# Kernel tuning notes

Measured on AMD Instinct MI355X. Metric: run time of the kernel, lower is better.

## Reference

```python
import jax, jax.numpy as jnp
import numpy as np

N_IN, N_H0, N_H1, N_H2, N_H3, N_OUT = 512, 1024, 1024, 1024, 512, 128
B, T = 128, 512
STD = 0.05


def setup_inputs() -> dict:
    key = jax.random.key(0)
    ks = jax.random.split(key, 7)
    # torch nn.Linear(in, out, bias=False) stores weight as [out, in]
    return {
        "input_spikes": jax.random.uniform(ks[0], (B, T, N_IN), dtype=jnp.float32),
        "W_in_h0": STD * jax.random.normal(ks[1], (N_H0, N_IN), dtype=jnp.float32),
        "W_h0_h1": STD * jax.random.normal(ks[2], (N_H1, N_H0), dtype=jnp.float32),
        "W_h1_h2": STD * jax.random.normal(ks[3], (N_H2, N_H1), dtype=jnp.float32),
        "W_h2_h2": STD * jax.random.normal(ks[4], (N_H2, N_H2), dtype=jnp.float32),
        "W_h2_h3": STD * jax.random.normal(ks[5], (N_H3, N_H2), dtype=jnp.float32),
        "W_h3_out": STD * jax.random.normal(ks[6], (N_OUT, N_H3), dtype=jnp.float32),
    }


def _lif(current, v, alpha, v_th):
    v = alpha * v + current
    s = (v >= v_th).astype(v.dtype)
    return s, v * (1.0 - s)


def reference(input_spikes, W_in_h0, W_h0_h1, W_h1_h2, W_h2_h2, W_h2_h3, W_h3_out):
    b = input_spikes.shape[0]
    dt = input_spikes.dtype
    z = lambda n: jnp.zeros((b, n), dtype=dt)
    # carry: membrane potentials for h0..h3, out, plus recurrent h2 spikes
    init = (z(N_H0), z(N_H1), z(N_H2), z(N_H3), z(N_OUT), z(N_H2))
    xs = jnp.swapaxes(input_spikes, 0, 1)  # [T, B, N_IN]

    def step(carry, x_t):
        v0, v1, v2, v3, vo, s2_prev = carry
        s0, v0 = _lif(x_t @ W_in_h0.T, v0, 0.9, 0.5)
        s1, v1 = _lif(s0 @ W_h0_h1.T, v1, 0.95, 0.5)
        s2, v2 = _lif(s1 @ W_h1_h2.T + s2_prev @ W_h2_h2.T, v2, 0.93, 0.5)
        s3, v3 = _lif(s2 @ W_h2_h3.T, v3, 0.9, 0.5)
        so, vo = _lif(s3 @ W_h3_out.T, vo, 0.82, 0.8)
        return (v0, v1, v2, v3, vo, s2), so

    _, out = jax.lax.scan(step, init, xs)
    output_spikes = jnp.swapaxes(out, 0, 1)  # [B, T, N_OUT]
    spike_counts = output_spikes.sum(axis=1)  # [B, N_OUT]
    return output_spikes, spike_counts
```

## Files before the change

kernel.cpp:

```cpp
#include <hip/hip_runtime.h>
#include <cstddef>


#define NB 128
#define NT 512

enum : size_t {
  OFF_V0   = 0,
  OFF_V1   = OFF_V0 + 131072,
  OFF_V2   = OFF_V1 + 131072,
  OFF_V3   = OFF_V2 + 131072,
  OFF_VO   = OFF_V3 + 65536,
  OFF_CNT  = OFF_VO + 16384,
  OFF_C2A  = OFF_CNT + 16384,
  OFF_BYTE = OFF_C2A + 262144,
  WS_FLOATS = OFF_BYTE + 229376
};
#define BS0 0
#define BS1 262144
#define BS2 524288
#define BS3 786432

__global__ __launch_bounds__(256) void init_kernel(float* __restrict__ wf) {
  size_t i = (size_t)blockIdx.x * blockDim.x + threadIdx.x;
  size_t stride = (size_t)gridDim.x * blockDim.x;
  for (size_t j = i; j < WS_FLOATS; j += stride) wf[j] = 0.0f;
}

template<bool ABYTE>
__device__ __forceinline__ void gemm_core(
    const void* __restrict__ Abase, int Astride,
    const float* __restrict__ W, int K, int fold,
    int bBase, int oBase,
    float (&As)[2][32][34], float (&Ws)[2][32][34],
    float acc[2][2])
{
  const int tid = threadIdx.x;
  const int ldRow = tid >> 3;
  const int ldK   = (tid & 7) << 2;
  const int tb = (tid & 15) << 1;
  const int to = (tid >> 4) << 1;

  const float* Wrow = W + (size_t)(oBase + ldRow) * K + ldK;
  const unsigned char* Abrow = nullptr;
  const float* Afrow = nullptr;
  if (ABYTE) Abrow = (const unsigned char*)Abase + (size_t)(bBase + ldRow) * Astride + ldK;
  else       Afrow = (const float*)Abase + (size_t)(bBase + ldRow) * Astride + ldK;

  const int NKT = K >> 5;

  float pa[4]; float4 pw;
  {
    float c0, c1, c2, c3;
    if (ABYTE) {
      unsigned int u = *(const unsigned int*)(Abrow);
      c0 = (float)(u & 0xff); c1 = (float)((u >> 8) & 0xff);
      c2 = (float)((u >> 16) & 0xff); c3 = (float)(u >> 24);
    } else {
      float4 f = *(const float4*)(Afrow);
      c0 = f.x; c1 = f.y; c2 = f.z; c3 = f.w;
    }
    float4 cw = *(const float4*)(Wrow);
    As[0][ldK + 0][ldRow] = c0; As[0][ldK + 1][ldRow] = c1;
    As[0][ldK + 2][ldRow] = c2; As[0][ldK + 3][ldRow] = c3;
    Ws[0][ldK + 0][ldRow] = cw.x; Ws[0][ldK + 1][ldRow] = cw.y;
    Ws[0][ldK + 2][ldRow] = cw.z; Ws[0][ldK + 3][ldRow] = cw.w;
  }
  if (NKT > 1) {
    if (ABYTE) {
      unsigned int u = *(const unsigned int*)(Abrow + 32);
      pa[0] = (float)(u & 0xff); pa[1] = (float)((u >> 8) & 0xff);
      pa[2] = (float)((u >> 16) & 0xff); pa[3] = (float)(u >> 24);
    } else {
      float4 f = *(const float4*)(Afrow + 32);
      pa[0] = f.x; pa[1] = f.y; pa[2] = f.z; pa[3] = f.w;
    }
    pw = *(const float4*)(Wrow + 32);
  }
  __syncthreads();

  float tot[2][2] = {{0.f, 0.f}, {0.f, 0.f}};
  float pan[2][2] = {{0.f, 0.f}, {0.f, 0.f}};
  int cb = 0;
  for (int kt = 0; kt < NKT; ++kt) {
    float na[4]; float4 nw;
    if (kt + 2 < NKT) {
      const int ko = (kt + 2) << 5;
      if (ABYTE) {
        unsigned int u = *(const unsigned int*)(Abrow + ko);
        na[0] = (float)(u & 0xff); na[1] = (float)((u >> 8) & 0xff);
        na[2] = (float)((u >> 16) & 0xff); na[3] = (float)(u >> 24);
      } else {
        float4 f = *(const float4*)(Afrow + ko);
        na[0] = f.x; na[1] = f.y; na[2] = f.z; na[3] = f.w;
      }
      nw = *(const float4*)(Wrow + ko);
    }
    if (fold && kt == 16) {
#pragma unroll
      for (int i = 0; i < 2; ++i)
#pragma unroll
        for (int j = 0; j < 2; ++j) {
          tot[i][j] = __fadd_rn(tot[i][j], pan[i][j]);
          pan[i][j] = 0.f;
        }
    }
#pragma unroll
    for (int k = 0; k < 32; ++k) {
      const float2 a = *(const float2*)&As[cb][k][tb];
      const float2 w = *(const float2*)&Ws[cb][k][to];
      pan[0][0] = fmaf(a.x, w.x, pan[0][0]);
      pan[0][1] = fmaf(a.x, w.y, pan[0][1]);
      pan[1][0] = fmaf(a.y, w.x, pan[1][0]);
      pan[1][1] = fmaf(a.y, w.y, pan[1][1]);
    }
    if (kt + 1 < NKT) {
      const int nb = cb ^ 1;
      As[nb][ldK + 0][ldRow] = pa[0]; As[nb][ldK + 1][ldRow] = pa[1];
      As[nb][ldK + 2][ldRow] = pa[2]; As[nb][ldK + 3][ldRow] = pa[3];
      Ws[nb][ldK + 0][ldRow] = pw.x; Ws[nb][ldK + 1][ldRow] = pw.y;
      Ws[nb][ldK + 2][ldRow] = pw.z; Ws[nb][ldK + 3][ldRow] = pw.w;
    }
    if (kt + 2 < NKT) { pa[0] = na[0]; pa[1] = na[1]; pa[2] = na[2]; pa[3] = na[3]; pw = nw; }
    __syncthreads();
    cb ^= 1;
  }
#pragma unroll
  for (int i = 0; i < 2; ++i)
#pragma unroll
    for (int j = 0; j < 2; ++j)
      acc[i][j] = __fadd_rn(tot[i][j], pan[i][j]);
}

__global__ __launch_bounds__(256) void phase_kernel(
    const float* __restrict__ x,
    const float* __restrict__ W0, const float* __restrict__ W1,
    const float* __restrict__ W2a, const float* __restrict__ W2b,
    const float* __restrict__ W3, const float* __restrict__ W4,
    float* __restrict__ wf, float* __restrict__ out, int p)
{
  float* cnt = wf + OFF_CNT;
  float* c2a = wf + OFF_C2A;
  unsigned char* sb = (unsigned char*)(wf + OFF_BYTE);
  const int cur = p & 1, prev = cur ^ 1;

  const int blk = blockIdx.x;
  int g, lb, t, K, N, fold;
  if (blk < 128)      { g = 0; lb = blk;       t = p;     K = 512;  N = 1024; fold = 0; }
  else if (blk < 256) { g = 1; lb = blk - 128; t = p - 1; K = 1024; N = 1024; fold = 1; }
  else if (blk < 384) { g = 2; lb = blk - 256; t = p - 2; K = 1024; N = 1024; fold = 1; }
  else if (blk < 512) { g = 3; lb = blk - 384; t = p - 3; K = 1024; N = 1024; fold = 1; }
  else if (blk < 576) { g = 4; lb = blk - 512; t = p - 4; K = 1024; N = 512;  fold = 1; }
  else                { g = 5; lb = blk - 576; t = p - 5; K = 512;  N = 128;  fold = 0; }
  if (t < 0 || t >= NT) return;

  const int ntO = N >> 5;
  const int bBase = (lb / ntO) << 5;
  const int oBase = (lb % ntO) << 5;

  const float* Wm; const void* Ab; int Astride;
  switch (g) {
    case 0: Wm = W0;  Ab = x + (size_t)t * 512;              Astride = NT * 512; break;
    case 1: Wm = W1;  Ab = sb + BS1 - BS1 + (size_t)prev * 131072; Astride = 1024; break;
    case 2: Wm = W2a; Ab = sb + BS1 + (size_t)prev * 131072; Astride = 1024; break;
    case 3: Wm = W2b; Ab = sb + BS2 + (size_t)prev * 131072; Astride = 1024; break;
    case 4: Wm = W3;  Ab = sb + BS2 + (size_t)prev * 131072; Astride = 1024; break;
    default: Wm = W4; Ab = sb + BS3 + (size_t)prev * 65536;  Astride = 512;  break;
  }

  __shared__ float As[2][32][34];
  __shared__ float Ws[2][32][34];
  float acc[2][2];
  if (g == 0) gemm_core<false>(Ab, Astride, Wm, K, fold, bBase, oBase, As, Ws, acc);
  else        gemm_core<true >(Ab, Astride, Wm, K, fold, bBase, oBase, As, Ws, acc);

  const int tid = threadIdx.x;
  const int tb = (tid & 15) << 1;
  const int to = (tid >> 4) << 1;

  if (g == 2) {
    float* dst = c2a + (size_t)cur * 131072;
#pragma unroll
    for (int i = 0; i < 2; ++i) {
      const int b = bBase + tb + i;
      float2 st; st.x = acc[i][0]; st.y = acc[i][1];
      *(float2*)(dst + (size_t)b * 1024 + oBase + to) = st;
    }
    return;
  }

  float alpha, vth = 0.5f;
  float* v; unsigned char* sOut = nullptr;
  switch (g) {
    case 0: alpha = 0.90f; v = wf + OFF_V0; sOut = sb + BS0 + (size_t)cur * 131072; break;
    case 1: alpha = 0.95f; v = wf + OFF_V1; sOut = sb + BS1 + (size_t)cur * 131072; break;
    case 3: alpha = 0.93f; v = wf + OFF_V2; sOut = sb + BS2 + (size_t)cur * 131072; break;
    case 4: alpha = 0.90f; v = wf + OFF_V3; sOut = sb + BS3 + (size_t)cur * 65536;  break;
    default: alpha = 0.82f; vth = 0.8f; v = wf + OFF_VO; break;
  }
  const float* c2aPrev = c2a + (size_t)prev * 131072;

#pragma unroll
  for (int i = 0; i < 2; ++i) {
    const int b = bBase + tb + i;
    int si[2];
#pragma unroll
    for (int j = 0; j < 2; ++j) {
      const int o = oBase + to + j;
      float cin = acc[i][j];
      if (g == 3)
        cin = __fadd_rn(c2aPrev[(size_t)b * 1024 + o], acc[i][j]);
      float* vp = v + (size_t)b * N + o;
      float vv = __fadd_rn(__fmul_rn(alpha, *vp), cin);
      int s = (vv >= vth) ? 1 : 0;
      float sf = (float)s;
      *vp = __fmul_rn(vv, __fsub_rn(1.0f, sf));
      si[j] = s;
      if (g == 5) {
        out[(size_t)b * (NT * 128) + (size_t)t * 128 + o] = sf;
        cnt[b * 128 + o] = __fadd_rn(cnt[b * 128 + o], sf);
      }
    }
    if (g != 5) {
      *(unsigned short*)(sOut + (size_t)b * N + oBase + to) =
          (unsigned short)(si[0] | (si[1] << 8));
    }
  }
}

__global__ __launch_bounds__(256) void fin_kernel(const float* __restrict__ counts,
                                                  float* __restrict__ out) {
  int i = blockIdx.x * blockDim.x + threadIdx.x;
  if (i < 128 * 128) out[(size_t)128 * NT * 128 + i] = counts[i];
}

extern "C" void kernel_launch(void* const* d_in, const int* in_sizes, int n_in,
                              void* d_out, int out_size, void* d_ws, size_t ws_size,
                              hipStream_t stream) {
  const float* x   = (const float*)d_in[0];
  const float* W0  = (const float*)d_in[1];
  const float* W1  = (const float*)d_in[2];
  const float* W2a = (const float*)d_in[3];
  const float* W2b = (const float*)d_in[4];
  const float* W3  = (const float*)d_in[5];
  const float* W4  = (const float*)d_in[6];
  float* wf  = (float*)d_ws;
  float* out = (float*)d_out;

  init_kernel<<<512, 256, 0, stream>>>(wf);
  for (int p = 0; p < NT + 5; ++p) {
    phase_kernel<<<592, 256, 0, stream>>>(x, W0, W1, W2a, W2b, W3, W4, wf, out, p);
  }
  fin_kernel<<<64, 256, 0, stream>>>(wf + OFF_CNT, out);
}
```

Measured before the change: 24.21 ms.

## Replace per-timestep launches with persistent kernel and grid-wide barrier

Replaces the 517 per-phase kernel launches with one persistent 512-block kernel that loops over phases, synchronising all blocks through a flag-based grid barrier in global memory. Membrane potentials and spike counts stay in LDS per thread instead of being read and written to global memory each step. Work is retiled: layer-0 uses 32x64 tiles with the small output layer merged into the same blocks, and the 1024-K GEMMs split K across two 128-thread halves that are reduced in LDS. This removes launch overhead and global state traffic, but depends on all 512 blocks being co-resident, which is checked with an occupancy query before falling back to a multi-launch path.

```diff
diff --git a/kernel.cpp b/kernel.cpp
--- a/kernel.cpp
+++ b/kernel.cpp
@@ -4,6 +4,7 @@
 
 #define NB 128
 #define NT 512
+#define NBLK 512
 
 enum : size_t {
   OFF_V0   = 0,
@@ -14,218 +15,444 @@
   OFF_CNT  = OFF_VO + 16384,
   OFF_C2A  = OFF_CNT + 16384,
   OFF_BYTE = OFF_C2A + 262144,
-  WS_FLOATS = OFF_BYTE + 229376
+  WS_FLOATS = OFF_BYTE + 229376,
+  OFF_ARR  = WS_FLOATS,
+  OFF_FLAGF = OFF_ARR + 8192,
+  WS_TOTAL = OFF_FLAGF + 16
 };
 #define BS0 0
 #define BS1 262144
 #define BS2 524288
 #define BS3 786432
 
+__device__ __forceinline__ void st_u16_agent(unsigned char* p, unsigned short v) {
+  __hip_atomic_store((unsigned short*)p, v, __ATOMIC_RELAXED, __HIP_MEMORY_SCOPE_AGENT);
+}
+__device__ __forceinline__ unsigned long long ld_u64_agent(const unsigned char* p) {
+  return __hip_atomic_load((const unsigned long long*)p, __ATOMIC_RELAXED, __HIP_MEMORY_SCOPE_AGENT);
+}
+__device__ __forceinline__ void st_u64_agent(void* p, unsigned long long v) {
+  __hip_atomic_store((unsigned long long*)p, v, __ATOMIC_RELAXED, __HIP_MEMORY_SCOPE_AGENT);
+}
+__device__ __forceinline__ unsigned long long ld_u64_agentf(const float* p) {
+  return __hip_atomic_load((const unsigned long long*)p, __ATOMIC_RELAXED, __HIP_MEMORY_SCOPE_AGENT);
+}
+__device__ __forceinline__ unsigned ld_u32_agent(const unsigned* p) {
+  return __hip_atomic_load(p, __ATOMIC_RELAXED, __HIP_MEMORY_SCOPE_AGENT);
+}
+__device__ __forceinline__ void st_u32_agent(unsigned* p, unsigned v) {
+  __hip_atomic_store(p, v, __ATOMIC_RELAXED, __HIP_MEMORY_SCOPE_AGENT);
+}
+
+union F2U { float2 f; unsigned long long u; };
+
+__device__ __forceinline__ void unpack8(unsigned long long v, float* f) {
+  unsigned lo = (unsigned)v, hi = (unsigned)(v >> 32);
+  f[0] = (float)(lo & 0xff); f[1] = (float)((lo >> 8) & 0xff);
+  f[2] = (float)((lo >> 16) & 0xff); f[3] = (float)(lo >> 24);
+  f[4] = (float)(hi & 0xff); f[5] = (float)((hi >> 8) & 0xff);
+  f[6] = (float)((hi >> 16) & 0xff); f[7] = (float)(hi >> 24);
+}
+
+__device__ __forceinline__ void gemm_split32(
+    const unsigned char* __restrict__ Abase,
+    const float* __restrict__ W,
+    int bBase, int oBase, int grp, int lt,
+    float* AsG, float* WsG, float acc[4][2])
+{
+  const int ar = lt >> 2, ac = (lt & 3) << 3;
+  const int wr = lt >> 2, wk = (lt & 3) << 3;
+  const int tb4 = (lt >> 4) << 2;
+  const int to2 = (lt & 15) << 1;
+  const int kb = grp << 9;
+
+  const unsigned char* Arow = Abase + (size_t)(bBase + ar) * 1024 + kb + ac;
+  const float* Wr = W + (size_t)(oBase + wr) * 1024 + kb + wk;
+
+  {
+    float a[8]; unpack8(ld_u64_agent(Arow), a);
+    float4 w0 = *(const float4*)(Wr);
+    float4 w1 = *(const float4*)(Wr + 4);
+#pragma unroll
+    for (int i = 0; i < 8; ++i) AsG[(ac + i) * 32 + ar] = a[i];
+    WsG[(wk+0)*36+wr] = w0.x; WsG[(wk+1)*36+wr] = w0.y;
+    WsG[(wk+2)*36+wr] = w0.z; WsG[(wk+3)*36+wr] = w0.w;
+    WsG[(wk+4)*36+wr] = w1.x; WsG[(wk+5)*36+wr] = w1.y;
+    WsG[(wk+6)*36+wr] = w1.z; WsG[(wk+7)*36+wr] = w1.w;
+  }
+  unsigned long long pa = ld_u64_agent(Arow + 32);
+  float4 pw0 = *(const float4*)(Wr + 32);
+  float4 pw1 = *(const float4*)(Wr + 36);
+  __syncthreads();
+
+  int cb = 0;
+#pragma unroll 1
+  for (int kt = 0; kt < 16; ++kt) {
+    unsigned long long na; float4 nw0, nw1;
+    if (kt + 2 < 16) {
+      const int ko = (kt + 2) << 5;
+      na  = ld_u64_agent(Arow + ko);
+      nw0 = *(const float4*)(Wr + ko);
+      nw1 = *(const float4*)(Wr + ko + 4);
+    }
+    const float* Asb = AsG + cb * 1024;
+    const float* Wsb = WsG + cb * 1152;
+#pragma unroll
+    for (int k = 0; k < 32; ++k) {
+      const float4 a = *(const float4*)&Asb[k * 32 + tb4];
+      const float2 w = *(const float2*)&Wsb[k * 36 + to2];
+      acc[0][0] = fmaf(a.x, w.x, acc[0][0]);
+      acc[0][1] = fmaf(a.x, w.y, acc[0][1]);
+      acc[1][0] = fmaf(a.y, w.x, acc[1][0]);
+      acc[1][1] = fmaf(a.y, w.y, acc[1][1]);
+      acc[2][0] = fmaf(a.z, w.x, acc[2][0]);
+      acc[2][1] = fmaf(a.z, w.y, acc[2][1]);
+      acc[3][0] = fmaf(a.w, w.x, acc[3][0]);
+      acc[3][1] = fmaf(a.w, w.y, acc[3][1]);
+    }
+    if (kt + 1 < 16) {
+      float* Asn = AsG + (cb ^ 1) * 1024;
+      float* Wsn = WsG + (cb ^ 1) * 1152;
+      float a[8]; unpack8(pa, a);
+#pragma unroll
+      for (int i = 0; i < 8; ++i) Asn[(ac + i) * 32 + ar] = a[i];
+      Wsn[(wk+0)*36+wr] = pw0.x; Wsn[(wk+1)*36+wr] = pw0.y;
+      Wsn[(wk+2)*36+wr] = pw0.z; Wsn[(wk+3)*36+wr] = pw0.w;
+      Wsn[(wk+4)*36+wr] = pw1.x; Wsn[(wk+5)*36+wr] = pw1.y;
+      Wsn[(wk+6)*36+wr] = pw1.z; Wsn[(wk+7)*36+wr] = pw1.w;
+    }
+    if (kt + 2 < 16) { pa = na; pw0 = nw0; pw1 = nw1; }
+    __syncthreads();
+    cb ^= 1;
+  }
+}
+
+__device__ __forceinline__ void gemm_x64(
+    const float* __restrict__ xrow,
+    const float* __restrict__ W,
+    int bBase, int oBase, int tid,
+    float* As, float* Ws, float acc[4][2])
+{
+  const int ar = tid >> 3, ac4 = (tid & 7) << 2;
+  const int wr = tid >> 2, wk = (tid & 3) << 3;
+  const int tb4 = (tid >> 5) << 2;
+  const int to2 = (tid & 31) << 1;
+  const float* Af = xrow + (size_t)(bBase + ar) * (NT * 512) + ac4;
+  const float* Wr = W + (size_t)(oBase + wr) * 512 + wk;
+
+  {
+    float4 a = *(const float4*)Af;
+    float4 w0 = *(const float4*)Wr;
+    float4 w1 = *(const float4*)(Wr + 4);
+    As[(ac4+0)*32+ar] = a.x; As[(ac4+1)*32+ar] = a.y;
+    As[(ac4+2)*32+ar] = a.z; As[(ac4+3)*32+ar] = a.w;
+    Ws[(wk+0)*68+wr] = w0.x; Ws[(wk+1)*68+wr] = w0.y;
+    Ws[(wk+2)*68+wr] = w0.z; Ws[(wk+3)*68+wr] = w0.w;
+    Ws[(wk+4)*68+wr] = w1.x; Ws[(wk+5)*68+wr] = w1.y;
+    Ws[(wk+6)*68+wr] = w1.z; Ws[(wk+7)*68+wr] = w1.w;
+  }
+  float4 paf = *(const float4*)(Af + 32);
+  float4 pw0 = *(const float4*)(Wr + 32);
+  float4 pw1 = *(const float4*)(Wr + 36);
+  __syncthreads();
+
+  int cb = 0;
+#pragma unroll 1
+  for (int kt = 0; kt < 16; ++kt) {
+    float4 naf, nw0, nw1;
+    if (kt + 2 < 16) {
+      const int ko = (kt + 2) << 5;
+      naf = *(const float4*)(Af + ko);
+      nw0 = *(const float4*)(Wr + ko);
+      nw1 = *(const float4*)(Wr + ko + 4);
+    }
+    const float* Asb = As + cb * 1024;
+    const float* Wsb = Ws + cb * 2176;
+#pragma unroll
+    for (int k = 0; k < 32; ++k) {
+      const float4 a = *(const float4*)&Asb[k * 32 + tb4];
+      const float2 w = *(const float2*)&Wsb[k * 68 + to2];
+      acc[0][0] = fmaf(a.x, w.x, acc[0][0]);
+      acc[0][1] = fmaf(a.x, w.y, acc[0][1]);
+      acc[1][0] = fmaf(a.y, w.x, acc[1][0]);
+      acc[1][1] = fmaf(a.y, w.y, acc[1][1]);
+      acc[2][0] = fmaf(a.z, w.x, acc[2][0]);
+      acc[2][1] = fmaf(a.z, w.y, acc[2][1]);
+      acc[3][0] = fmaf(a.w, w.x, acc[3][0]);
+      acc[3][1] = fmaf(a.w, w.y, acc[3][1]);
+    }
+    if (kt + 1 < 16) {
+      float* Asn = As + (cb ^ 1) * 1024;
+      float* Wsn = Ws + (cb ^ 1) * 2176;
+      Asn[(ac4+0)*32+ar] = paf.x; Asn[(ac4+1)*32+ar] = paf.y;
+      Asn[(ac4+2)*32+ar] = paf.z; Asn[(ac4+3)*32+ar] = paf.w;
+      Wsn[(wk+0)*68+wr] = pw0.x; Wsn[(wk+1)*68+wr] = pw0.y;
+      Wsn[(wk+2)*68+wr] = pw0.z; Wsn[(wk+3)*68+wr] = pw0.w;
+      Wsn[(wk+4)*68+wr] = pw1.x; Wsn[(wk+5)*68+wr] = pw1.y;
+      Wsn[(wk+6)*68+wr] = pw1.z; Wsn[(wk+7)*68+wr] = pw1.w;
+    }
+    if (kt + 2 < 16) { paf = naf; pw0 = nw0; pw1 = nw1; }
+    __syncthreads();
+    cb ^= 1;
+  }
+}
+
+template<bool PERSIST>
+__device__ __forceinline__ void do_phase512(
+    int g, int lb, int p,
+    const float* __restrict__ x,
+    const float* __restrict__ W0, const float* __restrict__ W1,
+    const float* __restrict__ W2a, const float* __restrict__ W2b,
+    const float* __restrict__ W3, const float* __restrict__ W4,
+    float* __restrict__ wf, float* __restrict__ out,
+    float* AsB, float* WsB, float* vpriv)
+{
+  unsigned char* sb = (unsigned char*)(wf + OFF_BYTE);
+  float* c2a = wf + OFF_C2A;
+  const int cur = p & 1, prev = cur ^ 1;
+  const int tid = threadIdx.x;
+
+  if (g == 0) {
+    const int t0 = p;
+    if (t0 < NT) {
+      const int bBase = (lb >> 4) << 5;
+      const int oBase = (lb & 15) << 6;
+      float acc[4][2] = {{0.f,0.f},{0.f,0.f},{0.f,0.f},{0.f,0.f}};
+      gemm_x64(x + (size_t)t0 * 512, W0, bBase, oBase, tid, AsB, WsB, acc);
+      const int tb4 = (tid >> 5) << 2, to2 = (tid & 31) << 1;
+      unsigned char* sOut = sb + BS0 + (size_t)cur * 131072;
+      float* vg = wf + OFF_V0;
+#pragma unroll
+      for (int i = 0; i < 4; ++i) {
+        const int b = bBase + tb4 + i;
+        int si[2];
+#pragma unroll
+        for (int j = 0; j < 2; ++j) {
+          const int o = oBase + to2 + j;
+          float vold = PERSIST ? vpriv[i*2+j] : vg[(size_t)b*1024 + o];
+          float vv = __fadd_rn(__fmul_rn(0.90f, vold), acc[i][j]);
+          int s = (vv >= 0.5f) ? 1 : 0;
+          float sf = (float)s;
+          float nv = __fmul_rn(vv, __fsub_rn(1.0f, sf));
+          if (PERSIST) vpriv[i*2+j] = nv; else vg[(size_t)b*1024 + o] = nv;
+          si[j] = s;
+        }
+        st_u16_agent(sOut + (size_t)b * 1024 + oBase + to2,
+                     (unsigned short)(si[0] | (si[1] << 8)));
+      }
+    }
+    const int t4 = p - 5;
+    if (t4 >= 0 && t4 < NT) {
+      const int b4 = ((lb >> 4) << 5) + (tid >> 3);
+      const int o4 = ((lb & 15) << 3) + (tid & 7);
+      const unsigned char* a3 = sb + BS3 + (size_t)prev * 65536 + (size_t)b4 * 512;
+      const float* w4r = W4 + (size_t)o4 * 512;
+      float acc = 0.f;
+#pragma unroll 4
+      for (int kk = 0; kk < 512; kk += 8) {
+        float a[8]; unpack8(ld_u64_agent(a3 + kk), a);
+        float4 wA = *(const float4*)(w4r + kk);
+        float4 wB = *(const float4*)(w4r + kk + 4);
+        acc = fmaf(a[0], wA.x, acc);
+        acc = fmaf(a[1], wA.y, acc);
+        acc = fmaf(a[2], wA.z, acc);
+        acc = fmaf(a[3], wA.w, acc);
+        acc = fmaf(a[4], wB.x, acc);
+        acc = fmaf(a[5], wB.y, acc);
+        acc = fmaf(a[6], wB.z, acc);
+        acc = fmaf(a[7], wB.w, acc);
+      }
+      float vold = PERSIST ? vpriv[8] : wf[OFF_VO + b4 * 128 + o4];
+      float vv = __fadd_rn(__fmul_rn(0.82f, vold), acc);
+      int s = (vv >= 0.8f) ? 1 : 0;
+      float sf = (float)s;
+      float nv = __fmul_rn(vv, __fsub_rn(1.0f, sf));
+      if (PERSIST) vpriv[8] = nv; else wf[OFF_VO + b4 * 128 + o4] = nv;
+      out[(size_t)b4 * (NT * 128) + (size_t)t4 * 128 + o4] = sf;
+      if (PERSIST) vpriv[9] = __fadd_rn(vpriv[9], sf);
+      else wf[OFF_CNT + b4 * 128 + o4] = __fadd_rn(wf[OFF_CNT + b4 * 128 + o4], sf);
+    }
+    return;
+  }
+
+  const int dt = (g == 1) ? 1 : (g == 2) ? 2 : (g == 3) ? 3 : 4;
+  const int t = p - dt;
+  if (t < 0 || t >= NT) return;
+
+  const unsigned char* Ab; const float* Wm;
+  switch (g) {
+    case 1:  Ab = sb + BS0 + (size_t)prev * 131072; Wm = W1;  break;
+    case 2:  Ab = sb + BS1 + (size_t)prev * 131072; Wm = W2a; break;
+    case 3:  Ab = sb + BS2 + (size_t)prev * 131072; Wm = W2b; break;
+    default: Ab = sb + BS2 + (size_t)prev * 131072; Wm = W3;  break;
+  }
+  const int ntO = (g == 4) ? 16 : 32;
+  const int N   = (g == 4) ? 512 : 1024;
+  const int bBase = (lb / ntO) << 5;
+  const int oBase = (lb % ntO) << 5;
+  const int grp = tid >> 7, lt = tid & 127;
+
+  float acc[4][2] = {{0.f,0.f},{0.f,0.f},{0.f,0.f},{0.f,0.f}};
+  gemm_split32(Ab, Wm, bBase, oBase, grp, lt,
+               AsB + grp * 2048, WsB + grp * 2304, acc);
+
+  float* foldp = AsB + 2048;
+  if (grp == 1) {
+    float4 h0, h1;
+    h0.x = acc[0][0]; h0.y = acc[0][1]; h0.z = acc[1][0]; h0.w = acc[1][1];
+    h1.x = acc[2][0]; h1.y = acc[2][1]; h1.z = acc[3][0]; h1.w = acc[3][1];
+    *(float4*)(foldp + lt * 8) = h0;
+    *(float4*)(foldp + lt * 8 + 4) = h1;
+  }
+  __syncthreads();
+  if (grp == 0) {
+    float4 h0 = *(const float4*)(foldp + lt * 8);
+    float4 h1 = *(const float4*)(foldp + lt * 8 + 4);
+    acc[0][0] = __fadd_rn(acc[0][0], h0.x); acc[0][1] = __fadd_rn(acc[0][1], h0.y);
+    acc[1][0] = __fadd_rn(acc[1][0], h0.z); acc[1][1] = __fadd_rn(acc[1][1], h0.w);
+    acc[2][0] = __fadd_rn(acc[2][0], h1.x); acc[2][1] = __fadd_rn(acc[2][1], h1.y);
+    acc[3][0] = __fadd_rn(acc[3][0], h1.z); acc[3][1] = __fadd_rn(acc[3][1], h1.w);
+
+    const int tb4 = (lt >> 4) << 2, to2 = (lt & 15) << 1;
+    if (g == 2) {
+      float* dst = c2a + (size_t)cur * 131072;
+#pragma unroll
+      for (int i = 0; i < 4; ++i) {
+        const int b = bBase + tb4 + i;
+        F2U u; u.f.x = acc[i][0]; u.f.y = acc[i][1];
+        st_u64_agent(dst + (size_t)b * 1024 + oBase + to2, u.u);
+      }
+    } else {
+      float alpha; float* vg; unsigned char* sOut;
+      if (g == 1)      { alpha = 0.95f; vg = wf + OFF_V1; sOut = sb + BS1 + (size_t)cur * 131072; }
+      else if (g == 3) { alpha = 0.93f; vg = wf + OFF_V2; sOut = sb + BS2 + (size_t)cur * 131072; }
+      else             { alpha = 0.90f; vg = wf + OFF_V3; sOut = sb + BS3 + (size_t)cur * 65536;  }
+      const float* c2aPrev = c2a + (size_t)prev * 131072;
+#pragma unroll
+      for (int i = 0; i < 4; ++i) {
+        const int b = bBase + tb4 + i;
+        float cin[2];
+        if (g == 3) {
+          F2U u; u.u = ld_u64_agentf(c2aPrev + (size_t)b * 1024 + oBase + to2);
+          cin[0] = __fadd_rn(u.f.x, acc[i][0]);
+          cin[1] = __fadd_rn(u.f.y, acc[i][1]);
+        } else {
+          cin[0] = acc[i][0]; cin[1] = acc[i][1];
+        }
+        int si[2];
+#pragma unroll
+        for (int j = 0; j < 2; ++j) {
+          const int o = oBase + to2 + j;
+          float vold = PERSIST ? vpriv[i*2+j] : vg[(size_t)b * N + o];
+          float vv = __fadd_rn(__fmul_rn(alpha, vold), cin[j]);
+          int s = (vv >= 0.5f) ? 1 : 0;
+          float sf = (float)s;
+          float nv = __fmul_rn(vv, __fsub_rn(1.0f, sf));
+          if (PERSIST) vpriv[i*2+j] = nv; else vg[(size_t)b * N + o] = nv;
+          si[j] = s;
+        }
+        st_u16_agent(sOut + (size_t)b * N + oBase + to2,
+                     (unsigned short)(si[0] | (si[1] << 8)));
+      }
+    }
+  }
+}
+
+__device__ __forceinline__ void phase_barrier(int p, unsigned* arr, unsigned* flag) {
+  const int tid = threadIdx.x;
+  __syncthreads();
+  const unsigned tgt = (unsigned)(p + 1);
+  if (blockIdx.x == 0) {
+    if (tid == 0) st_u32_agent(arr, tgt);
+    int ok;
+    do {
+      unsigned a0 = ld_u32_agent(arr + (tid * 2) * 16);
+      unsigned a1 = ld_u32_agent(arr + (tid * 2 + 1) * 16);
+      ok = __syncthreads_and((int)(a0 >= tgt && a1 >= tgt));
+      if (!ok) __builtin_amdgcn_s_sleep(1);
+    } while (!ok);
+    if (tid == 0) st_u32_agent(flag, tgt);
+    __syncthreads();
+  } else {
+    if (tid == 0) {
+      st_u32_agent(arr + blockIdx.x * 16, tgt);
+      while (ld_u32_agent(flag) < tgt) __builtin_amdgcn_s_sleep(2);
+    }
+    __syncthreads();
+  }
+}
+
+__global__ __launch_bounds__(256) void pre_kernel(float* __restrict__ wf) {
+  size_t i = (size_t)blockIdx.x * blockDim.x + threadIdx.x;
+  size_t stride = (size_t)gridDim.x * blockDim.x;
+  for (size_t j = i; j < WS_TOTAL; j += stride) wf[j] = 0.0f;
+}
+
+__global__ __launch_bounds__(256, 2) void persist3(
+    const float* __restrict__ x,
+    const float* __restrict__ W0, const float* __restrict__ W1,
+    const float* __restrict__ W2a, const float* __restrict__ W2b,
+    const float* __restrict__ W3, const float* __restrict__ W4,
+    float* __restrict__ wf, float* __restrict__ out)
+{
+  __shared__ float AsB[4096];
+  __shared__ float WsB[4608];
+  __shared__ float vLds[256][11];
+  const int tid = threadIdx.x;
+  float* vpriv = &vLds[tid][0];
+#pragma unroll
+  for (int i = 0; i < 11; ++i) vpriv[i] = 0.0f;
+
+  unsigned* arr  = (unsigned*)(wf + OFF_ARR);
+  unsigned* flag = (unsigned*)(wf + OFF_FLAGF);
+
+  const int blk = blockIdx.x;
+  int g, lb;
+  if (blk < 64)       { g = 0; lb = blk; }
+  else if (blk < 192) { g = 1; lb = blk - 64; }
+  else if (blk < 320) { g = 2; lb = blk - 192; }
+  else if (blk < 448) { g = 3; lb = blk - 320; }
+  else                { g = 4; lb = blk - 448; }
+
+  for (int p = 0; p < NT + 5; ++p) {
+    do_phase512<true>(g, lb, p, x, W0, W1, W2a, W2b, W3, W4, wf, out,
+                      AsB, WsB, vpriv);
+    phase_barrier(p, arr, flag);
+  }
+
+  if (g == 0) {
+    const int b4 = ((lb >> 4) << 5) + (tid >> 3);
+    const int o4 = ((lb & 15) << 3) + (tid & 7);
+    out[(size_t)128 * NT * 128 + (size_t)b4 * 128 + o4] = vpriv[9];
+  }
+}
+
+
 __global__ __launch_bounds__(256) void init_kernel(float* __restrict__ wf) {
   size_t i = (size_t)blockIdx.x * blockDim.x + threadIdx.x;
   size_t stride = (size_t)gridDim.x * blockDim.x;
-  for (size_t j = i; j < WS_FLOATS; j += stride) wf[j] = 0.0f;
-}
-
-template<bool ABYTE>
-__device__ __forceinline__ void gemm_core(
-    const void* __restrict__ Abase, int Astride,
-    const float* __restrict__ W, int K, int fold,
-    int bBase, int oBase,
-    float (&As)[2][32][34], float (&Ws)[2][32][34],
-    float acc[2][2])
-{
-  const int tid = threadIdx.x;
-  const int ldRow = tid >> 3;
-  const int ldK   = (tid & 7) << 2;
-  const int tb = (tid & 15) << 1;
-  const int to = (tid >> 4) << 1;
-
-  const float* Wrow = W + (size_t)(oBase + ldRow) * K + ldK;
-  const unsigned char* Abrow = nullptr;
-  const float* Afrow = nullptr;
-  if (ABYTE) Abrow = (const unsigned char*)Abase + (size_t)(bBase + ldRow) * Astride + ldK;
-  else       Afrow = (const float*)Abase + (size_t)(bBase + ldRow) * Astride + ldK;
-
-  const int NKT = K >> 5;
-
-  float pa[4]; float4 pw;
-  {
-    float c0, c1, c2, c3;
-    if (ABYTE) {
-      unsigned int u = *(const unsigned int*)(Abrow);
-      c0 = (float)(u & 0xff); c1 = (float)((u >> 8) & 0xff);
-      c2 = (float)((u >> 16) & 0xff); c3 = (float)(u >> 24);
-    } else {
-      float4 f = *(const float4*)(Afrow);
-      c0 = f.x; c1 = f.y; c2 = f.z; c3 = f.w;
-    }
-    float4 cw = *(const float4*)(Wrow);
-    As[0][ldK + 0][ldRow] = c0; As[0][ldK + 1][ldRow] = c1;
-    As[0][ldK + 2][ldRow] = c2; As[0][ldK + 3][ldRow] = c3;
-    Ws[0][ldK + 0][ldRow] = cw.x; Ws[0][ldK + 1][ldRow] = cw.y;
-    Ws[0][ldK + 2][ldRow] = cw.z; Ws[0][ldK + 3][ldRow] = cw.w;
-  }
-  if (NKT > 1) {
-    if (ABYTE) {
-      unsigned int u = *(const unsigned int*)(Abrow + 32);
-      pa[0] = (float)(u & 0xff); pa[1] = (float)((u >> 8) & 0xff);
-      pa[2] = (float)((u >> 16) & 0xff); pa[3] = (float)(u >> 24);
-    } else {
-      float4 f = *(const float4*)(Afrow + 32);
-      pa[0] = f.x; pa[1] = f.y; pa[2] = f.z; pa[3] = f.w;
-    }
-    pw = *(const float4*)(Wrow + 32);
-  }
-  __syncthreads();
-
-  float tot[2][2] = {{0.f, 0.f}, {0.f, 0.f}};
-  float pan[2][2] = {{0.f, 0.f}, {0.f, 0.f}};
-  int cb = 0;
-  for (int kt = 0; kt < NKT; ++kt) {
-    float na[4]; float4 nw;
-    if (kt + 2 < NKT) {
-      const int ko = (kt + 2) << 5;
-      if (ABYTE) {
-        unsigned int u = *(const unsigned int*)(Abrow + ko);
-        na[0] = (float)(u & 0xff); na[1] = (float)((u >> 8) & 0xff);
-        na[2] = (float)((u >> 16) & 0xff); na[3] = (float)(u >> 24);
-      } else {
-        float4 f = *(const float4*)(Afrow + ko);
-        na[0] = f.x; na[1] = f.y; na[2] = f.z; na[3] = f.w;
-      }
-      nw = *(const float4*)(Wrow + ko);
-    }
-    if (fold && kt == 16) {
-#pragma unroll
-      for (int i = 0; i < 2; ++i)
-#pragma unroll
-        for (int j = 0; j < 2; ++j) {
-          tot[i][j] = __fadd_rn(tot[i][j], pan[i][j]);
-          pan[i][j] = 0.f;
-        }
-    }
-#pragma unroll
-    for (int k = 0; k < 32; ++k) {
-      const float2 a = *(const float2*)&As[cb][k][tb];
-      const float2 w = *(const float2*)&Ws[cb][k][to];
-      pan[0][0] = fmaf(a.x, w.x, pan[0][0]);
-      pan[0][1] = fmaf(a.x, w.y, pan[0][1]);
-      pan[1][0] = fmaf(a.y, w.x, pan[1][0]);
-      pan[1][1] = fmaf(a.y, w.y, pan[1][1]);
-    }
-    if (kt + 1 < NKT) {
-      const int nb = cb ^ 1;
-      As[nb][ldK + 0][ldRow] = pa[0]; As[nb][ldK + 1][ldRow] = pa[1];
-      As[nb][ldK + 2][ldRow] = pa[2]; As[nb][ldK + 3][ldRow] = pa[3];
-      Ws[nb][ldK + 0][ldRow] = pw.x; Ws[nb][ldK + 1][ldRow] = pw.y;
-      Ws[nb][ldK + 2][ldRow] = pw.z; Ws[nb][ldK + 3][ldRow] = pw.w;
-    }
-    if (kt + 2 < NKT) { pa[0] = na[0]; pa[1] = na[1]; pa[2] = na[2]; pa[3] = na[3]; pw = nw; }
-    __syncthreads();
-    cb ^= 1;
-  }
-#pragma unroll
-  for (int i = 0; i < 2; ++i)
-#pragma unroll
-    for (int j = 0; j < 2; ++j)
-      acc[i][j] = __fadd_rn(tot[i][j], pan[i][j]);
-}
-
-__global__ __launch_bounds__(256) void phase_kernel(
+  for (size_t j = i; j < WS_TOTAL; j += stride) wf[j] = 0.0f;
+}
+
+__global__ __launch_bounds__(256) void phase_kernel512(
     const float* __restrict__ x,
     const float* __restrict__ W0, const float* __restrict__ W1,
     const float* __restrict__ W2a, const float* __restrict__ W2b,
     const float* __restrict__ W3, const float* __restrict__ W4,
     float* __restrict__ wf, float* __restrict__ out, int p)
 {
-  float* cnt = wf + OFF_CNT;
-  float* c2a = wf + OFF_C2A;
-  unsigned char* sb = (unsigned char*)(wf + OFF_BYTE);
-  const int cur = p & 1, prev = cur ^ 1;
-
+  __shared__ float AsB[4096];
+  __shared__ float WsB[4608];
   const int blk = blockIdx.x;
-  int g, lb, t, K, N, fold;
-  if (blk < 128)      { g = 0; lb = blk;       t = p;     K = 512;  N = 1024; fold = 0; }
-  else if (blk < 256) { g = 1; lb = blk - 128; t = p - 1; K = 1024; N = 1024; fold = 1; }
-  else if (blk < 384) { g = 2; lb = blk - 256; t = p - 2; K = 1024; N = 1024; fold = 1; }
-  else if (blk < 512) { g = 3; lb = blk - 384; t = p - 3; K = 1024; N = 1024; fold = 1; }
-  else if (blk < 576) { g = 4; lb = blk - 512; t = p - 4; K = 1024; N = 512;  fold = 1; }
-  else                { g = 5; lb = blk - 576; t = p - 5; K = 512;  N = 128;  fold = 0; }
-  if (t < 0 || t >= NT) return;
-
-  const int ntO = N >> 5;
-  const int bBase = (lb / ntO) << 5;
-  const int oBase = (lb % ntO) << 5;
-
-  const float* Wm; const void* Ab; int Astride;
-  switch (g) {
-    case 0: Wm = W0;  Ab = x + (size_t)t * 512;              Astride = NT * 512; break;
-    case 1: Wm = W1;  Ab = sb + BS1 - BS1 + (size_t)prev * 131072; Astride = 1024; break;
-    case 2: Wm = W2a; Ab = sb + BS1 + (size_t)prev * 131072; Astride = 1024; break;
-    case 3: Wm = W2b; Ab = sb + BS2 + (size_t)prev * 131072; Astride = 1024; break;
-    case 4: Wm = W3;  Ab = sb + BS2 + (size_t)prev * 131072; Astride = 1024; break;
-    default: Wm = W4; Ab = sb + BS3 + (size_t)prev * 65536;  Astride = 512;  break;
-  }
-
-  __shared__ float As[2][32][34];
-  __shared__ float Ws[2][32][34];
-  float acc[2][2];
-  if (g == 0) gemm_core<false>(Ab, Astride, Wm, K, fold, bBase, oBase, As, Ws, acc);
-  else        gemm_core<true >(Ab, Astride, Wm, K, fold, bBase, oBase, As, Ws, acc);
-
-  const int tid = threadIdx.x;
-  const int tb = (tid & 15) << 1;
-  const int to = (tid >> 4) << 1;
-
-  if (g == 2) {
-    float* dst = c2a + (size_t)cur * 131072;
-#pragma unroll
-    for (int i = 0; i < 2; ++i) {
-      const int b = bBase + tb + i;
-      float2 st; st.x = acc[i][0]; st.y = acc[i][1];
-      *(float2*)(dst + (size_t)b * 1024 + oBase + to) = st;
-    }
-    return;
-  }
-
-  float alpha, vth = 0.5f;
-  float* v; unsigned char* sOut = nullptr;
-  switch (g) {
-    case 0: alpha = 0.90f; v = wf + OFF_V0; sOut = sb + BS0 + (size_t)cur * 131072; break;
-    case 1: alpha = 0.95f; v = wf + OFF_V1; sOut = sb + BS1 + (size_t)cur * 131072; break;
-    case 3: alpha = 0.93f; v = wf + OFF_V2; sOut = sb + BS2 + (size_t)cur * 131072; break;
-    case 4: alpha = 0.90f; v = wf + OFF_V3; sOut = sb + BS3 + (size_t)cur * 65536;  break;
-    default: alpha = 0.82f; vth = 0.8f; v = wf + OFF_VO; break;
-  }
-  const float* c2aPrev = c2a + (size_t)prev * 131072;
-
-#pragma unroll
-  for (int i = 0; i < 2; ++i) {
-    const int b = bBase + tb + i;
-    int si[2];
-#pragma unroll
-    for (int j = 0; j < 2; ++j) {
-      const int o = oBase + to + j;
-      float cin = acc[i][j];
-      if (g == 3)
-        cin = __fadd_rn(c2aPrev[(size_t)b * 1024 + o], acc[i][j]);
-      float* vp = v + (size_t)b * N + o;
-      float vv = __fadd_rn(__fmul_rn(alpha, *vp), cin);
-      int s = (vv >= vth) ? 1 : 0;
-      float sf = (float)s;
-      *vp = __fmul_rn(vv, __fsub_rn(1.0f, sf));
-      si[j] = s;
-      if (g == 5) {
-        out[(size_t)b * (NT * 128) + (size_t)t * 128 + o] = sf;
-        cnt[b * 128 + o] = __fadd_rn(cnt[b * 128 + o], sf);
-      }
-    }
-    if (g != 5) {
-      *(unsigned short*)(sOut + (size_t)b * N + oBase + to) =
-          (unsigned short)(si[0] | (si[1] << 8));
-    }
-  }
+  int g, lb;
+  if (blk < 64)       { g = 0; lb = blk; }
+  else if (blk < 192) { g = 1; lb = blk - 64; }
+  else if (blk < 320) { g = 2; lb = blk - 192; }
+  else if (blk < 448) { g = 3; lb = blk - 320; }
+  else                { g = 4; lb = blk - 448; }
+  float vd[11];
+  do_phase512<false>(g, lb, p, x, W0, W1, W2a, W2b, W3, W4, wf, out,
+                     AsB, WsB, vd);
 }
 
 __global__ __launch_bounds__(256) void fin_kernel(const float* __restrict__ counts,
@@ -233,6 +460,7 @@
   int i = blockIdx.x * blockDim.x + threadIdx.x;
   if (i < 128 * 128) out[(size_t)128 * NT * 128 + i] = counts[i];
 }
+
 
 extern "C" void kernel_launch(void* const* d_in, const int* in_sizes, int n_in,
                               void* d_out, int out_size, void* d_ws, size_t ws_size,
@@ -247,9 +475,21 @@
   float* wf  = (float*)d_ws;
   float* out = (float*)d_out;
 
-  init_kernel<<<512, 256, 0, stream>>>(wf);
-  for (int p = 0; p < NT + 5; ++p) {
-    phase_kernel<<<592, 256, 0, stream>>>(x, W0, W1, W2a, W2b, W3, W4, wf, out, p);
-  }
-  fin_kernel<<<64, 256, 0, stream>>>(wf + OFF_CNT, out);
-}
+  int maxBlocksPerCU = 0;
+  hipError_t qe = hipOccupancyMaxActiveBlocksPerMultiprocessor(
+      &maxBlocksPerCU, persist3, 256, 0);
+  const bool wsOK = ws_size >= WS_TOTAL * sizeof(float);
+
+  if (qe == hipSuccess && maxBlocksPerCU >= 2 && wsOK) {
+    pre_kernel<<<256, 256, 0, stream>>>(wf);
+    persist3<<<NBLK, 256, 0, stream>>>(x, W0, W1, W2a, W2b, W3, W4, wf, out);
+  } else {
+    (void)hipGetLastError();
+    init_kernel<<<512, 256, 0, stream>>>(wf);
+    for (int p = 0; p < NT + 5; ++p) {
+      phase_kernel512<<<NBLK, 256, 0, stream>>>(x, W0, W1, W2a, W2b, W3, W4,
+                                                wf, out, p);
+    }
+    fin_kernel<<<64, 256, 0, stream>>>(wf + OFF_CNT, out);
+  }
+}
```

Measured after the change: 19.65 ms. -18.8%, faster.
